# Optimization experiments

Measured on AMD Instinct MI355X. Metric: run time of the kernel, lower is better.

The kernel has to match this reference:

```python
import jax, jax.numpy as jnp
import numpy as np

N = 20000        # graph_node_num
C = 512          # cluster_num
E = 640000       # num edges (avg degree 32)
NFEAT = 128


def _gcn(x, W, b, edge_index, n):
    # PyG GCNConv: add self-loops, symmetric deg^-1/2 normalization, h = x @ W.T, bias after aggregation
    loop = jnp.arange(n, dtype=edge_index.dtype)
    src = jnp.concatenate([edge_index[0], loop])
    dst = jnp.concatenate([edge_index[1], loop])
    deg = jax.ops.segment_sum(jnp.ones_like(dst, x.dtype), dst, num_segments=n)
    dinv = jax.lax.rsqrt(jnp.maximum(deg, 1.0))  # deg >= 1 due to self-loops
    norm = dinv[src] * dinv[dst]                 # [E+n]
    h = x @ W.T                                  # [n, out]
    out = jax.ops.segment_sum(norm[:, None] * h[src], dst, num_segments=n)
    return out + b


def setup_inputs() -> dict:
    rng = np.random.default_rng(0)
    key = jax.random.key(0)
    edge = rng.integers(0, N, size=(2, E), dtype=np.int32)
    cluster = rng.integers(0, C, size=(N,), dtype=np.int32)
    # avg_pool coarsening of edge_index: remap to cluster ids, drop self-loops, coalesce (dedupe)
    cs, cd = cluster[edge[0]], cluster[edge[1]]
    m = cs != cd
    pairs = np.unique(cs[m].astype(np.int64) * C + cd[m].astype(np.int64))
    coarse_edge = np.stack([pairs // C, pairs % C]).astype(np.int32)

    ks = jax.random.split(key, 16)

    def w(k, o, i):
        return (jax.random.normal(k, (o, i), jnp.float32) / np.sqrt(i)).astype(jnp.float32)

    return {
        "x": jax.random.normal(ks[0], (N, NFEAT), jnp.float32),
        "W_G1": w(ks[1], 64, NFEAT), "b_G1": jnp.zeros((64,), jnp.float32),
        "Wf_G1": w(ks[2], 128, 64), "bf_G1": jnp.zeros((128,), jnp.float32),
        "W_G2": w(ks[3], 256, 128), "b_G2": jnp.zeros((256,), jnp.float32),
        "Wf_G2": w(ks[4], 256, 256), "bf_G2": jnp.zeros((256,), jnp.float32),
        "W_L1": w(ks[5], 128, 256), "b_L1": jnp.zeros((128,), jnp.float32),
        "Wf_L1": w(ks[6], 96, 128), "bf_L1": jnp.zeros((96,), jnp.float32),
        "W_L2": w(ks[7], 64, 96), "b_L2": jnp.zeros((64,), jnp.float32),
        "Wf_L2": w(ks[8], 32, 64), "bf_L2": jnp.zeros((32,), jnp.float32),
        "W_M1": w(ks[9], 16, 32), "b_M1": jnp.zeros((16,), jnp.float32),
        "Wf_M1": w(ks[10], 8, 16), "bf_M1": jnp.zeros((8,), jnp.float32),
        "W_O1": w(ks[11], 5, 8), "b_O1": jnp.zeros((5,), jnp.float32),
        "W_fcO": w(ks[12], 3 * N, 5 * C),  # fc_O1, bias=False
        "edge_index": jnp.asarray(edge),
        "cluster": jnp.asarray(cluster),
        "in_batch": jnp.zeros((N,), jnp.int32),
        "coarse_edge_index": jnp.asarray(coarse_edge),
    }


def reference(x, W_G1, b_G1, Wf_G1, bf_G1, W_G2, b_G2, Wf_G2, bf_G2,
              W_L1, b_L1, Wf_L1, bf_L1, W_L2, b_L2, Wf_L2, bf_L2,
              W_M1, b_M1, Wf_M1, bf_M1, W_O1, b_O1, W_fcO,
              edge_index, cluster, in_batch, coarse_edge_index):
    elu = jax.nn.elu
    x = elu(_gcn(x, W_G1, b_G1, edge_index, N))
    x = elu(x @ Wf_G1.T + bf_G1)
    x = elu(_gcn(x, W_G2, b_G2, edge_index, N))
    x = elu(x @ Wf_G2.T + bf_G2)
    # InstanceNorm(256), no batch arg -> single graph, per-channel over nodes, no affine
    mu = x.mean(axis=0)
    var = x.var(axis=0)
    y = (x - mu) * jax.lax.rsqrt(var + 1e-5)
    # avg_pool over clusters (batch_num=1 -> batch_cluster == cluster)
    bc = cluster + in_batch * C
    cnt = jax.ops.segment_sum(jnp.ones((N,), y.dtype), bc, num_segments=C)
    cx = jax.ops.segment_sum(y, bc, num_segments=C) / jnp.maximum(cnt, 1.0)[:, None]
    z = elu(_gcn(cx, W_L1, b_L1, coarse_edge_index, C))
    z = elu(z @ Wf_L1.T + bf_L1)
    z = elu(_gcn(z, W_L2, b_L2, coarse_edge_index, C))
    z = elu(z @ Wf_L2.T + bf_L2)
    z = elu(_gcn(z, W_M1, b_M1, coarse_edge_index, C))
    z = elu(z @ Wf_M1.T + bf_M1)
    g_feat = _gcn(z, W_O1, b_O1, coarse_edge_index, C).reshape(-1)  # [5*C]
    o_feat = W_fcO @ g_feat                                        # [3*N]
    return (g_feat, o_feat)
```

## Files before the change

kernel.cpp:

```cpp
#include <hip/hip_runtime.h>
#include <math.h>

#define NN 20000
#define CC 512

__device__ __forceinline__ float eluf(float x) { return x > 0.f ? x : __expf(x) - 1.f; }

__global__ void k_zero(float4* __restrict__ p, int n4) {
  int i = blockIdx.x * blockDim.x + threadIdx.x;
  if (i < n4) p[i] = make_float4(0.f, 0.f, 0.f, 0.f);
}

__global__ void k_count3(const int* __restrict__ dstF, int nF, int* __restrict__ cF,
                         const int* __restrict__ dstC, int nC, int* __restrict__ cC,
                         const int* __restrict__ clus, int nK, int* __restrict__ cK) {
  int i = blockIdx.x * blockDim.x + threadIdx.x;
  if (i < nF) { atomicAdd(&cF[dstF[i]], 1); return; }
  i -= nF;
  if (i < nC) { atomicAdd(&cC[dstC[i]], 1); return; }
  i -= nC;
  if (i < nK) atomicAdd(&cK[clus[i]], 1);
}

__global__ __launch_bounds__(1024) void k_scan3(
    const int* __restrict__ c0, int n0, int* __restrict__ r0, float* __restrict__ d0,
    const int* __restrict__ c1, int n1, int* __restrict__ r1, float* __restrict__ d1,
    const int* __restrict__ c2, int n2, int* __restrict__ r2) {
  const int* counts; int n; int* rowptr; float* dinv;
  if (blockIdx.x == 0) { counts = c0; n = n0; rowptr = r0; dinv = d0; }
  else if (blockIdx.x == 1) { counts = c1; n = n1; rowptr = r1; dinv = d1; }
  else { counts = c2; n = n2; rowptr = r2; dinv = nullptr; }
  __shared__ int part[1024];
  int tid = threadIdx.x;
  int chunk = (n + 1023) >> 10;
  int beg = tid * chunk;
  int fin = beg + chunk; if (fin > n) fin = n;
  int s = 0;
  for (int i = beg; i < fin; ++i) {
    int c = counts[i];
    s += c;
    if (dinv) dinv[i] = rsqrtf((float)(c + 1));
  }
  part[tid] = s;
  __syncthreads();
  for (int off = 1; off < 1024; off <<= 1) {
    int v = (tid >= off) ? part[tid - off] : 0;
    __syncthreads();
    part[tid] += v;
    __syncthreads();
  }
  int base = (tid == 0) ? 0 : part[tid - 1];
  for (int i = beg; i < fin; ++i) { rowptr[i] = base; base += counts[i]; }
  if (tid == 1023) rowptr[n] = part[1023];
}

__global__ void k_scatter3(
    const int* __restrict__ edgeF, int EF, const int* __restrict__ rowF, int* __restrict__ fillF,
    const float* __restrict__ dinvF, int* __restrict__ csrcF, float* __restrict__ cnormF,
    const int* __restrict__ edgeC, int EC, const int* __restrict__ rowC, int* __restrict__ fillC,
    const float* __restrict__ dinvC, int* __restrict__ csrcC, float* __restrict__ cnormC,
    const int* __restrict__ clus, int NK, const int* __restrict__ rowK, int* __restrict__ fillK,
    int* __restrict__ cnodes) {
  int i = blockIdx.x * blockDim.x + threadIdx.x;
  if (i < EF) {
    int d = edgeF[EF + i];
    int pos = rowF[d] + atomicAdd(&fillF[d], 1);
    int s = edgeF[i];
    csrcF[pos] = s;
    cnormF[pos] = dinvF[s] * dinvF[d];
    return;
  }
  i -= EF;
  if (i < EC) {
    int d = edgeC[EC + i];
    int pos = rowC[d] + atomicAdd(&fillC[d], 1);
    int s = edgeC[i];
    csrcC[pos] = s;
    cnormC[pos] = dinvC[s] * dinvC[d];
    return;
  }
  i -= EC;
  if (i < NK) {
    int d = clus[i];
    int pos = rowK[d] + atomicAdd(&fillK[d], 1);
    cnodes[pos] = i;
  }
}

__global__ __launch_bounds__(256) void k_gemm(const float* __restrict__ X,
                                              const float* __restrict__ W,
                                              const float* __restrict__ bias,
                                              float* __restrict__ Y,
                                              int nrows, int K, int outF, int act) {
  __shared__ float Xt[64][65];
  __shared__ float Wt[64][65];
  int row0 = blockIdx.x * 64;
  int col0 = blockIdx.y * 64;
  int tid = threadIdx.x;
  int cg = (tid & 15) * 4;
  int rg = (tid >> 4) * 4;
  float acc[4][4] = {};
  for (int kk = 0; kk < K; kk += 64) {
#pragma unroll
    for (int i = 0; i < 4; ++i) {
      int f = tid + 256 * i;
      int a = f >> 4;
      int kq = f & 15;
      int gk = kk + kq * 4;
      float4 xv = make_float4(0.f, 0.f, 0.f, 0.f);
      int gr = row0 + a;
      if (gr < nrows && gk < K) xv = *(const float4*)&X[(size_t)gr * K + gk];
      int kb = kq * 4;
      Xt[a][kb] = xv.x; Xt[a][kb + 1] = xv.y; Xt[a][kb + 2] = xv.z; Xt[a][kb + 3] = xv.w;
      float4 wv = make_float4(0.f, 0.f, 0.f, 0.f);
      int gc = col0 + a;
      if (gc < outF && gk < K) wv = *(const float4*)&W[(size_t)gc * K + gk];
      Wt[kb][a] = wv.x; Wt[kb + 1][a] = wv.y; Wt[kb + 2][a] = wv.z; Wt[kb + 3][a] = wv.w;
    }
    __syncthreads();
#pragma unroll 8
    for (int k = 0; k < 64; ++k) {
      float w0 = Wt[k][cg + 0], w1 = Wt[k][cg + 1], w2 = Wt[k][cg + 2], w3 = Wt[k][cg + 3];
      float x0 = Xt[rg + 0][k], x1 = Xt[rg + 1][k], x2 = Xt[rg + 2][k], x3 = Xt[rg + 3][k];
      acc[0][0] += x0 * w0; acc[0][1] += x0 * w1; acc[0][2] += x0 * w2; acc[0][3] += x0 * w3;
      acc[1][0] += x1 * w0; acc[1][1] += x1 * w1; acc[1][2] += x1 * w2; acc[1][3] += x1 * w3;
      acc[2][0] += x2 * w0; acc[2][1] += x2 * w1; acc[2][2] += x2 * w2; acc[2][3] += x2 * w3;
      acc[3][0] += x3 * w0; acc[3][1] += x3 * w1; acc[3][2] += x3 * w2; acc[3][3] += x3 * w3;
    }
    __syncthreads();
  }
#pragma unroll
  for (int i = 0; i < 4; ++i) {
    int gr = row0 + rg + i;
    if (gr >= nrows) continue;
#pragma unroll
    for (int j = 0; j < 4; ++j) {
      int gc = col0 + cg + j;
      if (gc >= outF) continue;
      float v = acc[i][j];
      if (bias) v += bias[gc];
      if (act) v = eluf(v);
      Y[(size_t)gr * outF + gc] = v;
    }
  }
}

__global__ __launch_bounds__(256) void k_gemm2(const float* __restrict__ X,
                                               const float* __restrict__ W,
                                               const float* __restrict__ bias,
                                               float* __restrict__ Y,
                                               int nrows, int K, int outF, int act) {
  __shared__ float Xt[32][132];
  __shared__ float Wt[32][68];
  int row0 = blockIdx.x * 128;
  int col0 = blockIdx.y * 64;
  int tid = threadIdx.x;
  int tc = (tid & 15) * 4;
  int tr = (tid >> 4) * 8;
  float acc[8][4] = {};
  for (int kk = 0; kk < K; kk += 32) {
#pragma unroll
    for (int i = 0; i < 4; ++i) {
      int f = tid + 256 * i;
      int r = f >> 3;
      int kq = f & 7;
      int gr = row0 + r;
      float4 v = make_float4(0.f, 0.f, 0.f, 0.f);
      if (gr < nrows) v = *(const float4*)&X[(size_t)gr * K + kk + kq * 4];
      int kb = kq * 4;
      Xt[kb][r] = v.x; Xt[kb + 1][r] = v.y; Xt[kb + 2][r] = v.z; Xt[kb + 3][r] = v.w;
    }
#pragma unroll
    for (int i = 0; i < 2; ++i) {
      int f = tid + 256 * i;
      int c = f >> 3;
      int kq = f & 7;
      int gc = col0 + c;
      float4 v = make_float4(0.f, 0.f, 0.f, 0.f);
      if (gc < outF) v = *(const float4*)&W[(size_t)gc * K + kk + kq * 4];
      int kb = kq * 4;
      Wt[kb][c] = v.x; Wt[kb + 1][c] = v.y; Wt[kb + 2][c] = v.z; Wt[kb + 3][c] = v.w;
    }
    __syncthreads();
#pragma unroll 8
    for (int k = 0; k < 32; ++k) {
      float4 w = *(const float4*)&Wt[k][tc];
      float4 xa = *(const float4*)&Xt[k][tr];
      float4 xb = *(const float4*)&Xt[k][tr + 4];
      float xs[8] = {xa.x, xa.y, xa.z, xa.w, xb.x, xb.y, xb.z, xb.w};
      float ws4[4] = {w.x, w.y, w.z, w.w};
#pragma unroll
      for (int i = 0; i < 8; ++i)
#pragma unroll
        for (int j = 0; j < 4; ++j) acc[i][j] += xs[i] * ws4[j];
    }
    __syncthreads();
  }
#pragma unroll
  for (int i = 0; i < 8; ++i) {
    int gr = row0 + tr + i;
    if (gr >= nrows) continue;
    int gc = col0 + tc;
    float4 v;
    v.x = acc[i][0]; v.y = acc[i][1]; v.z = acc[i][2]; v.w = acc[i][3];
    if (bias) { v.x += bias[gc]; v.y += bias[gc + 1]; v.z += bias[gc + 2]; v.w += bias[gc + 3]; }
    if (act) { v.x = eluf(v.x); v.y = eluf(v.y); v.z = eluf(v.z); v.w = eluf(v.w); }
    if (gc + 3 < outF) {
      *(float4*)&Y[(size_t)gr * outF + gc] = v;
    } else {
      float vs[4] = {v.x, v.y, v.z, v.w};
      for (int j = 0; j < 4; ++j)
        if (gc + j < outF) Y[(size_t)gr * outF + gc + j] = vs[j];
    }
  }
}

__global__ __launch_bounds__(256) void k_agg_fine64(
    const int* __restrict__ rowptr, const int* __restrict__ csrc, const float* __restrict__ cnorm,
    const float* __restrict__ h, const float* __restrict__ dinv, const float* __restrict__ bias,
    float* __restrict__ out, int n) {
  int w = blockIdx.x * 4 + (threadIdx.x >> 6);
  if (w >= n) return;
  int lane = threadIdx.x & 63;
  int start = rowptr[w], end = rowptr[w + 1];
  float acc = 0.f;
  int e = start;
  while (e < end && (e & 3)) { acc += cnorm[e] * h[(size_t)csrc[e] * 64 + lane]; ++e; }
  for (; e + 7 < end; e += 8) {
    int4 ia = *(const int4*)&csrc[e];
    int4 ib = *(const int4*)&csrc[e + 4];
    float4 na = *(const float4*)&cnorm[e];
    float4 nb = *(const float4*)&cnorm[e + 4];
    float v0 = h[(size_t)ia.x * 64 + lane];
    float v1 = h[(size_t)ia.y * 64 + lane];
    float v2 = h[(size_t)ia.z * 64 + lane];
    float v3 = h[(size_t)ia.w * 64 + lane];
    float v4 = h[(size_t)ib.x * 64 + lane];
    float v5 = h[(size_t)ib.y * 64 + lane];
    float v6 = h[(size_t)ib.z * 64 + lane];
    float v7 = h[(size_t)ib.w * 64 + lane];
    acc += na.x * v0 + na.y * v1 + na.z * v2 + na.w * v3 +
           nb.x * v4 + nb.y * v5 + nb.z * v6 + nb.w * v7;
  }
  for (; e < end; ++e) acc += cnorm[e] * h[(size_t)csrc[e] * 64 + lane];
  float dd = dinv[w]; dd *= dd;
  out[(size_t)w * 64 + lane] = eluf(acc + dd * h[(size_t)w * 64 + lane] + bias[lane]);
}

__global__ __launch_bounds__(256) void k_agg_fine128(
    const int* __restrict__ rowptr, const int* __restrict__ csrc, const float* __restrict__ cnorm,
    const float2* __restrict__ h2, const float* __restrict__ dinv,
    float2* __restrict__ out2, int n) {
  int w = blockIdx.x * 4 + (threadIdx.x >> 6);
  if (w >= n) return;
  int lane = threadIdx.x & 63;
  int start = rowptr[w], end = rowptr[w + 1];
  float ax = 0.f, ay = 0.f;
  int e = start;
  while (e < end && (e & 3)) {
    float nm = cnorm[e];
    float2 v = h2[(size_t)csrc[e] * 64 + lane];
    ax += nm * v.x; ay += nm * v.y; ++e;
  }
  for (; e + 7 < end; e += 8) {
    int4 ia = *(const int4*)&csrc[e];
    int4 ib = *(const int4*)&csrc[e + 4];
    float4 na = *(const float4*)&cnorm[e];
    float4 nb = *(const float4*)&cnorm[e + 4];
    float2 v0 = h2[(size_t)ia.x * 64 + lane];
    float2 v1 = h2[(size_t)ia.y * 64 + lane];
    float2 v2 = h2[(size_t)ia.z * 64 + lane];
    float2 v3 = h2[(size_t)ia.w * 64 + lane];
    float2 v4 = h2[(size_t)ib.x * 64 + lane];
    float2 v5 = h2[(size_t)ib.y * 64 + lane];
    float2 v6 = h2[(size_t)ib.z * 64 + lane];
    float2 v7 = h2[(size_t)ib.w * 64 + lane];
    ax += na.x * v0.x + na.y * v1.x + na.z * v2.x + na.w * v3.x +
          nb.x * v4.x + nb.y * v5.x + nb.z * v6.x + nb.w * v7.x;
    ay += na.x * v0.y + na.y * v1.y + na.z * v2.y + na.w * v3.y +
          nb.x * v4.y + nb.y * v5.y + nb.z * v6.y + nb.w * v7.y;
  }
  for (; e < end; ++e) {
    float nm = cnorm[e];
    float2 v = h2[(size_t)csrc[e] * 64 + lane];
    ax += nm * v.x; ay += nm * v.y;
  }
  float dd = dinv[w]; dd *= dd;
  float2 hw = h2[(size_t)w * 64 + lane];
  float2 o;
  o.x = ax + dd * hw.x;
  o.y = ay + dd * hw.y;
  out2[(size_t)w * 64 + lane] = o;
}

__global__ __launch_bounds__(256) void k_agg_coarse(int F,
    const int* __restrict__ rowptr, const int* __restrict__ csrc, const float* __restrict__ cnorm,
    const float* __restrict__ h, const float* __restrict__ dinv, const float* __restrict__ bias,
    float* __restrict__ out, int act) {
  int d = blockIdx.x;
  int lane = threadIdx.x & 63, wv = threadIdx.x >> 6;
  int start = rowptr[d], end = rowptr[d + 1];
  int cnt = end - start;
  int per = (cnt + 3) >> 2;
  int wbeg = start + wv * per;
  int wend = wbeg + per; if (wend > end) wend = end;
  float acc0 = 0.f, acc1 = 0.f;
  int e = wbeg;
  for (; e + 3 < wend; e += 4) {
    int s0 = csrc[e], s1 = csrc[e + 1], s2 = csrc[e + 2], s3 = csrc[e + 3];
    float n0 = cnorm[e], n1 = cnorm[e + 1], n2 = cnorm[e + 2], n3 = cnorm[e + 3];
    if (lane < F)
      acc0 += n0 * h[(size_t)s0 * F + lane] + n1 * h[(size_t)s1 * F + lane] +
              n2 * h[(size_t)s2 * F + lane] + n3 * h[(size_t)s3 * F + lane];
    if (lane + 64 < F)
      acc1 += n0 * h[(size_t)s0 * F + lane + 64] + n1 * h[(size_t)s1 * F + lane + 64] +
              n2 * h[(size_t)s2 * F + lane + 64] + n3 * h[(size_t)s3 * F + lane + 64];
  }
  for (; e < wend; ++e) {
    int s = csrc[e];
    float nm = cnorm[e];
    if (lane < F) acc0 += nm * h[(size_t)s * F + lane];
    if (lane + 64 < F) acc1 += nm * h[(size_t)s * F + lane + 64];
  }
  __shared__ float red[4][128];
  if (lane < F) red[wv][lane] = acc0;
  if (lane + 64 < F) red[wv][lane + 64] = acc1;
  __syncthreads();
  if (wv == 0) {
#pragma unroll 2
    for (int j = 0; j < 2; ++j) {
      int c = lane + j * 64;
      if (c < F) {
        float v = red[0][c] + red[1][c] + red[2][c] + red[3][c];
        float dd = dinv[d] * dinv[d];
        v += dd * h[(size_t)d * F + c] + bias[c];
        if (act) v = eluf(v);
        out[(size_t)d * F + c] = v;
      }
    }
  }
}

__global__ __launch_bounds__(256) void k_agg_coarse_fc2(int F,
    const int* __restrict__ rowptr, const int* __restrict__ csrc, const float* __restrict__ cnorm,
    const float* __restrict__ h, const float* __restrict__ dinv, const float* __restrict__ bias,
    const float* __restrict__ Wf, const float* __restrict__ bf, int outF2,
    const float* __restrict__ W2, int outF3,
    float* __restrict__ out) {
  int d = blockIdx.x;
  int lane = threadIdx.x & 63, wv = threadIdx.x >> 6;
  int start = rowptr[d], end = rowptr[d + 1];
  int cnt = end - start;
  int per = (cnt + 3) >> 2;
  int wbeg = start + wv * per;
  int wend = wbeg + per; if (wend > end) wend = end;
  float acc0 = 0.f, acc1 = 0.f;
  int e = wbeg;
  for (; e + 3 < wend; e += 4) {
    int s0 = csrc[e], s1 = csrc[e + 1], s2 = csrc[e + 2], s3 = csrc[e + 3];
    float n0 = cnorm[e], n1 = cnorm[e + 1], n2 = cnorm[e + 2], n3 = cnorm[e + 3];
    if (lane < F)
      acc0 += n0 * h[(size_t)s0 * F + lane] + n1 * h[(size_t)s1 * F + lane] +
              n2 * h[(size_t)s2 * F + lane] + n3 * h[(size_t)s3 * F + lane];
    if (lane + 64 < F)
      acc1 += n0 * h[(size_t)s0 * F + lane + 64] + n1 * h[(size_t)s1 * F + lane + 64] +
              n2 * h[(size_t)s2 * F + lane + 64] + n3 * h[(size_t)s3 * F + lane + 64];
  }
  for (; e < wend; ++e) {
    int s = csrc[e];
    float nm = cnorm[e];
    if (lane < F) acc0 += nm * h[(size_t)s * F + lane];
    if (lane + 64 < F) acc1 += nm * h[(size_t)s * F + lane + 64];
  }
  __shared__ float red[4][128];
  __shared__ __align__(16) float a_sh[128];
  __shared__ __align__(16) float z2_sh[96];
  if (lane < F) red[wv][lane] = acc0;
  if (lane + 64 < F) red[wv][lane + 64] = acc1;
  __syncthreads();
  if (wv == 0) {
#pragma unroll 2
    for (int j = 0; j < 2; ++j) {
      int c = lane + j * 64;
      if (c < F) {
        float v = red[0][c] + red[1][c] + red[2][c] + red[3][c];
        float dd = dinv[d] * dinv[d];
        a_sh[c] = eluf(v + dd * h[(size_t)d * F + c] + bias[c]);
      }
    }
  }
  __syncthreads();
  int j = threadIdx.x;
  if (j < outF2) {
    const float4* wr = (const float4*)(Wf + (size_t)j * F);
    const float4* ar = (const float4*)a_sh;
    float s = bf[j];
    for (int c = 0; c < (F >> 2); ++c) {
      float4 wv4 = wr[c];
      float4 av = ar[c];
      s += wv4.x * av.x + wv4.y * av.y + wv4.z * av.z + wv4.w * av.w;
    }
    z2_sh[j] = eluf(s);
  }
  __syncthreads();
  int m = threadIdx.x;
  if (m < outF3) {
    const float4* wr = (const float4*)(W2 + (size_t)m * outF2);
    const float4* zr = (const float4*)z2_sh;
    float s = 0.f;
    for (int c = 0; c < (outF2 >> 2); ++c) {
      float4 wv4 = wr[c];
      float4 zv = zr[c];
      s += wv4.x * zv.x + wv4.y * zv.y + wv4.z * zv.z + wv4.w * zv.w;
    }
    out[(size_t)d * outF3 + m] = s;
  }
}

__global__ __launch_bounds__(256) void k_chanstats(const float* __restrict__ x, int n,
                                                   float* __restrict__ s, float* __restrict__ s2) {
  int ch = threadIdx.x;
  float a = 0.f, b = 0.f;
  for (int r = blockIdx.x; r < n; r += gridDim.x) {
    float v = x[(size_t)r * 256 + ch];
    a += v;
    b += v * v;
  }
  atomicAdd(&s[ch], a);
  atomicAdd(&s2[ch], b);
}

__global__ __launch_bounds__(256) void k_pool(const float* __restrict__ x,
                                              const int* __restrict__ rowptr,
                                              const int* __restrict__ nodes,
                                              const float* __restrict__ sS,
                                              const float* __restrict__ sS2,
                                              float ninv,
                                              float* __restrict__ cx) {
  int c = blockIdx.x;
  int ch = threadIdx.x;
  float mu = sS[ch] * ninv;
  float var = sS2[ch] * ninv - mu * mu;
  float rstd = rsqrtf(var + 1e-5f);
  int start = rowptr[c], end = rowptr[c + 1];
  float s = 0.f;
  int i = start;
  for (; i + 3 < end; i += 4) {
    float v0 = x[(size_t)nodes[i] * 256 + ch];
    float v1 = x[(size_t)nodes[i + 1] * 256 + ch];
    float v2 = x[(size_t)nodes[i + 2] * 256 + ch];
    float v3 = x[(size_t)nodes[i + 3] * 256 + ch];
    s += v0 + v1 + v2 + v3;
  }
  for (; i < end; ++i) s += x[(size_t)nodes[i] * 256 + ch];
  int cnt = end - start; if (cnt < 1) cnt = 1;
  float v = s / (float)cnt;
  cx[(size_t)c * 256 + ch] = (v - mu) * rstd;
}

__global__ __launch_bounds__(256) void k_matvec(const float* __restrict__ W,
                                                const float* __restrict__ g,
                                                float* __restrict__ out, int M, int K) {
  __shared__ __align__(16) float gs[2560];
  for (int i = threadIdx.x; i < K; i += 256) gs[i] = g[i];
  __syncthreads();
  int lane = threadIdx.x & 63, wv = threadIdx.x >> 6;
#pragma unroll
  for (int rr = 0; rr < 4; ++rr) {
    int row = blockIdx.x * 16 + wv * 4 + rr;
    if (row >= M) break;
    const float4* Wr = (const float4*)(W + (size_t)row * K);
    float acc = 0.f;
#pragma unroll
    for (int it = 0; it < 10; ++it) {
      float4 w4 = Wr[it * 64 + lane];
      float4 g4 = *(const float4*)&gs[it * 256 + lane * 4];
      acc += w4.x * g4.x + w4.y * g4.y + w4.z * g4.z + w4.w * g4.w;
    }
#pragma unroll
    for (int off = 32; off; off >>= 1) acc += __shfl_down(acc, off, 64);
    if (lane == 0) out[row] = acc;
  }
}

extern "C" void kernel_launch(void* const* d_in, const int* in_sizes, int n_in,
                              void* d_out, int out_size, void* d_ws, size_t ws_size,
                              hipStream_t stream) {
  const float* x     = (const float*)d_in[0];
  const float* W_G1  = (const float*)d_in[1];
  const float* b_G1  = (const float*)d_in[2];
  const float* Wf_G1 = (const float*)d_in[3];
  const float* bf_G1 = (const float*)d_in[4];
  const float* W_G2  = (const float*)d_in[5];
  const float* b_G2  = (const float*)d_in[6];
  const float* Wf_G2 = (const float*)d_in[7];
  const float* bf_G2 = (const float*)d_in[8];
  const float* W_L1  = (const float*)d_in[9];
  const float* b_L1  = (const float*)d_in[10];
  const float* Wf_L1 = (const float*)d_in[11];
  const float* bf_L1 = (const float*)d_in[12];
  const float* W_L2  = (const float*)d_in[13];
  const float* b_L2  = (const float*)d_in[14];
  const float* Wf_L2 = (const float*)d_in[15];
  const float* bf_L2 = (const float*)d_in[16];
  const float* W_M1  = (const float*)d_in[17];
  const float* b_M1  = (const float*)d_in[18];
  const float* Wf_M1 = (const float*)d_in[19];
  const float* bf_M1 = (const float*)d_in[20];
  const float* W_O1  = (const float*)d_in[21];
  const float* b_O1  = (const float*)d_in[22];
  const float* W_fcO = (const float*)d_in[23];
  const int* edge    = (const int*)d_in[24];
  const int* cluster = (const int*)d_in[25];
  const int* cedge   = (const int*)d_in[27];

  const int E  = in_sizes[24] / 2;
  const int Ec = in_sizes[27] / 2;

  char* ws = (char*)d_ws;
  size_t off = 0;
  auto alloc = [&](size_t bytes) -> void* {
    void* p = ws + off;
    off = (off + bytes + 255) & ~(size_t)255;
    return p;
  };

  float* bufA = (float*)alloc((size_t)NN * 256 * 4);
  float* bufB = (float*)alloc((size_t)NN * 256 * 4);
  float* bufC = (float*)alloc((size_t)NN * 256 * 4);
  float* cx   = (float*)alloc((size_t)CC * 256 * 4);
  float* zA   = (float*)alloc((size_t)CC * 256 * 4);
  float* zB   = (float*)alloc((size_t)CC * 256 * 4);
  float* dinvF = (float*)alloc((size_t)NN * 4);
  float* dinvC = (float*)alloc((size_t)CC * 4);
  int* rowF  = (int*)alloc((size_t)(NN + 1) * 4);
  int* rowC  = (int*)alloc((size_t)(CC + 1) * 4);
  int* rowCl = (int*)alloc((size_t)(CC + 1) * 4);
  int* csrcF = (int*)alloc((size_t)E * 4);
  float* cnormF = (float*)alloc((size_t)E * 4);
  int* csrcC = (int*)alloc((size_t)Ec * 4);
  float* cnormC = (float*)alloc((size_t)Ec * 4);
  int* cnodes = (int*)alloc((size_t)NN * 4);
  size_t zoff = off;
  int* degF  = (int*)alloc((size_t)NN * 4);
  int* fillF = (int*)alloc((size_t)NN * 4);
  int* degC  = (int*)alloc((size_t)CC * 4);
  int* fillC = (int*)alloc((size_t)CC * 4);
  int* degCl = (int*)alloc((size_t)CC * 4);
  int* fillCl = (int*)alloc((size_t)CC * 4);
  float* chanS  = (float*)alloc(256 * 4);
  float* chanS2 = (float*)alloc(256 * 4);
  size_t zbytes = off - zoff;

  float* g_out = (float*)d_out;
  float* o_out = (float*)d_out + 2560;

  auto cdiv = [](int a, int b) { return (a + b - 1) / b; };

  k_zero<<<cdiv((int)(zbytes / 16), 256), 256, 0, stream>>>((float4*)(ws + zoff), (int)(zbytes / 16));

  k_count3<<<cdiv(E + Ec + NN, 256), 256, 0, stream>>>(edge + E, E, degF,
                                                       cedge + Ec, Ec, degC,
                                                       cluster, NN, degCl);
  k_scan3<<<3, 1024, 0, stream>>>(degF, NN, rowF, dinvF,
                                  degC, CC, rowC, dinvC,
                                  degCl, CC, rowCl);
  k_scatter3<<<cdiv(E + Ec + NN, 256), 256, 0, stream>>>(
      edge, E, rowF, fillF, dinvF, csrcF, cnormF,
      cedge, Ec, rowC, fillC, dinvC, csrcC, cnormC,
      cluster, NN, rowCl, fillCl, cnodes);

  k_gemm2<<<dim3(cdiv(NN, 128), 1), 256, 0, stream>>>(x, W_G1, nullptr, bufA, NN, 128, 64, 0);
  k_agg_fine64<<<NN / 4, 256, 0, stream>>>(rowF, csrcF, cnormF, bufA, dinvF, b_G1, bufC, NN);
  k_gemm2<<<dim3(cdiv(NN, 128), 2), 256, 0, stream>>>(bufC, Wf_G1, bf_G1, bufA, NN, 64, 128, 1);
  k_agg_fine128<<<NN / 4, 256, 0, stream>>>(rowF, csrcF, cnormF, (const float2*)bufA, dinvF,
                                            (float2*)bufC, NN);
  k_gemm2<<<dim3(cdiv(NN, 128), 4), 256, 0, stream>>>(bufC, W_G2, b_G2, bufB, NN, 128, 256, 1);
  k_gemm2<<<dim3(cdiv(NN, 128), 4), 256, 0, stream>>>(bufB, Wf_G2, bf_G2, bufA, NN, 256, 256, 1);

  k_chanstats<<<256, 256, 0, stream>>>(bufA, NN, chanS, chanS2);
  k_pool<<<CC, 256, 0, stream>>>(bufA, rowCl, cnodes, chanS, chanS2, 1.f / (float)NN, cx);

  k_gemm<<<dim3(8, 2), 256, 0, stream>>>(cx, W_L1, nullptr, zA, CC, 256, 128, 0);
  k_agg_coarse_fc2<<<CC, 256, 0, stream>>>(128, rowC, csrcC, cnormC, zA, dinvC, b_L1,
                                           Wf_L1, bf_L1, 96, W_L2, 64, zB);
  k_agg_coarse_fc2<<<CC, 256, 0, stream>>>(64, rowC, csrcC, cnormC, zB, dinvC, b_L2,
                                           Wf_L2, bf_L2, 32, W_M1, 16, zA);
  k_agg_coarse_fc2<<<CC, 256, 0, stream>>>(16, rowC, csrcC, cnormC, zA, dinvC, b_M1,
                                           Wf_M1, bf_M1, 8, W_O1, 5, zB);
  k_agg_coarse<<<CC, 256, 0, stream>>>(5, rowC, csrcC, cnormC, zB, dinvC, b_O1, g_out, 0);

  k_matvec<<<cdiv(3 * NN, 16), 256, 0, stream>>>(W_fcO, g_out, o_out, 3 * NN, 2560);
}
```

Baseline: 556.0 us.

## Split 128-wide fine aggregation into two passes and fuse pooling with L1 GEMM

The 128-feature fine aggregation now runs as two launches, each gathering one 64-column half of h, instead of one pass with float2 gathers. This shrinks the gathered working set per pass so it can stay resident in cache, at the price of reading the CSR indices and norms twice. Separately, the cluster pooling kernel now also computes the W_L1 projection per cluster row from shared memory, which removes the cx buffer and one tiny GEMM launch. Each pooling block re-reads all of W_L1 from global memory, and only half its threads do the matvec.

```diff
diff --git a/kernel.cpp b/kernel.cpp
--- a/kernel.cpp
+++ b/kernel.cpp
@@ -84,64 +84,6 @@
     int d = clus[i];
     int pos = rowK[d] + atomicAdd(&fillK[d], 1);
     cnodes[pos] = i;
-  }
-}
-
-__global__ __launch_bounds__(256) void k_gemm(const float* __restrict__ X,
-                                              const float* __restrict__ W,
-                                              const float* __restrict__ bias,
-                                              float* __restrict__ Y,
-                                              int nrows, int K, int outF, int act) {
-  __shared__ float Xt[64][65];
-  __shared__ float Wt[64][65];
-  int row0 = blockIdx.x * 64;
-  int col0 = blockIdx.y * 64;
-  int tid = threadIdx.x;
-  int cg = (tid & 15) * 4;
-  int rg = (tid >> 4) * 4;
-  float acc[4][4] = {};
-  for (int kk = 0; kk < K; kk += 64) {
-#pragma unroll
-    for (int i = 0; i < 4; ++i) {
-      int f = tid + 256 * i;
-      int a = f >> 4;
-      int kq = f & 15;
-      int gk = kk + kq * 4;
-      float4 xv = make_float4(0.f, 0.f, 0.f, 0.f);
-      int gr = row0 + a;
-      if (gr < nrows && gk < K) xv = *(const float4*)&X[(size_t)gr * K + gk];
-      int kb = kq * 4;
-      Xt[a][kb] = xv.x; Xt[a][kb + 1] = xv.y; Xt[a][kb + 2] = xv.z; Xt[a][kb + 3] = xv.w;
-      float4 wv = make_float4(0.f, 0.f, 0.f, 0.f);
-      int gc = col0 + a;
-      if (gc < outF && gk < K) wv = *(const float4*)&W[(size_t)gc * K + gk];
-      Wt[kb][a] = wv.x; Wt[kb + 1][a] = wv.y; Wt[kb + 2][a] = wv.z; Wt[kb + 3][a] = wv.w;
-    }
-    __syncthreads();
-#pragma unroll 8
-    for (int k = 0; k < 64; ++k) {
-      float w0 = Wt[k][cg + 0], w1 = Wt[k][cg + 1], w2 = Wt[k][cg + 2], w3 = Wt[k][cg + 3];
-      float x0 = Xt[rg + 0][k], x1 = Xt[rg + 1][k], x2 = Xt[rg + 2][k], x3 = Xt[rg + 3][k];
-      acc[0][0] += x0 * w0; acc[0][1] += x0 * w1; acc[0][2] += x0 * w2; acc[0][3] += x0 * w3;
-      acc[1][0] += x1 * w0; acc[1][1] += x1 * w1; acc[1][2] += x1 * w2; acc[1][3] += x1 * w3;
-      acc[2][0] += x2 * w0; acc[2][1] += x2 * w1; acc[2][2] += x2 * w2; acc[2][3] += x2 * w3;
-      acc[3][0] += x3 * w0; acc[3][1] += x3 * w1; acc[3][2] += x3 * w2; acc[3][3] += x3 * w3;
-    }
-    __syncthreads();
-  }
-#pragma unroll
-  for (int i = 0; i < 4; ++i) {
-    int gr = row0 + rg + i;
-    if (gr >= nrows) continue;
-#pragma unroll
-    for (int j = 0; j < 4; ++j) {
-      int gc = col0 + cg + j;
-      if (gc >= outF) continue;
-      float v = acc[i][j];
-      if (bias) v += bias[gc];
-      if (act) v = eluf(v);
-      Y[(size_t)gr * outF + gc] = v;
-    }
   }
 }
 
@@ -247,50 +189,37 @@
   out[(size_t)w * 64 + lane] = eluf(acc + dd * h[(size_t)w * 64 + lane] + bias[lane]);
 }
 
-__global__ __launch_bounds__(256) void k_agg_fine128(
+__global__ __launch_bounds__(256) void k_agg_fine128h(
     const int* __restrict__ rowptr, const int* __restrict__ csrc, const float* __restrict__ cnorm,
-    const float2* __restrict__ h2, const float* __restrict__ dinv,
-    float2* __restrict__ out2, int n) {
+    const float* __restrict__ h, const float* __restrict__ dinv,
+    float* __restrict__ out, int n, int half) {
   int w = blockIdx.x * 4 + (threadIdx.x >> 6);
   if (w >= n) return;
   int lane = threadIdx.x & 63;
+  const float* hh = h + half * 64 + lane;
   int start = rowptr[w], end = rowptr[w + 1];
-  float ax = 0.f, ay = 0.f;
+  float acc = 0.f;
   int e = start;
-  while (e < end && (e & 3)) {
-    float nm = cnorm[e];
-    float2 v = h2[(size_t)csrc[e] * 64 + lane];
-    ax += nm * v.x; ay += nm * v.y; ++e;
-  }
+  while (e < end && (e & 3)) { acc += cnorm[e] * hh[(size_t)csrc[e] * 128]; ++e; }
   for (; e + 7 < end; e += 8) {
     int4 ia = *(const int4*)&csrc[e];
     int4 ib = *(const int4*)&csrc[e + 4];
     float4 na = *(const float4*)&cnorm[e];
     float4 nb = *(const float4*)&cnorm[e + 4];
-    float2 v0 = h2[(size_t)ia.x * 64 + lane];
-    float2 v1 = h2[(size_t)ia.y * 64 + lane];
-    float2 v2 = h2[(size_t)ia.z * 64 + lane];
-    float2 v3 = h2[(size_t)ia.w * 64 + lane];
-    float2 v4 = h2[(size_t)ib.x * 64 + lane];
-    float2 v5 = h2[(size_t)ib.y * 64 + lane];
-    float2 v6 = h2[(size_t)ib.z * 64 + lane];
-    float2 v7 = h2[(size_t)ib.w * 64 + lane];
-    ax += na.x * v0.x + na.y * v1.x + na.z * v2.x + na.w * v3.x +
-          nb.x * v4.x + nb.y * v5.x + nb.z * v6.x + nb.w * v7.x;
-    ay += na.x * v0.y + na.y * v1.y + na.z * v2.y + na.w * v3.y +
-          nb.x * v4.y + nb.y * v5.y + nb.z * v6.y + nb.w * v7.y;
-  }
-  for (; e < end; ++e) {
-    float nm = cnorm[e];
-    float2 v = h2[(size_t)csrc[e] * 64 + lane];
-    ax += nm * v.x; ay += nm * v.y;
-  }
+    float v0 = hh[(size_t)ia.x * 128];
+    float v1 = hh[(size_t)ia.y * 128];
+    float v2 = hh[(size_t)ia.z * 128];
+    float v3 = hh[(size_t)ia.w * 128];
+    float v4 = hh[(size_t)ib.x * 128];
+    float v5 = hh[(size_t)ib.y * 128];
+    float v6 = hh[(size_t)ib.z * 128];
+    float v7 = hh[(size_t)ib.w * 128];
+    acc += na.x * v0 + na.y * v1 + na.z * v2 + na.w * v3 +
+           nb.x * v4 + nb.y * v5 + nb.z * v6 + nb.w * v7;
+  }
+  for (; e < end; ++e) acc += cnorm[e] * hh[(size_t)csrc[e] * 128];
   float dd = dinv[w]; dd *= dd;
-  float2 hw = h2[(size_t)w * 64 + lane];
-  float2 o;
-  o.x = ax + dd * hw.x;
-  o.y = ay + dd * hw.y;
-  out2[(size_t)w * 64 + lane] = o;
+  out[(size_t)w * 128 + half * 64 + lane] = acc + dd * hh[(size_t)w * 128];
 }
 
 __global__ __launch_bounds__(256) void k_agg_coarse(int F,
@@ -430,15 +359,17 @@
   atomicAdd(&s2[ch], b);
 }
 
-__global__ __launch_bounds__(256) void k_pool(const float* __restrict__ x,
-                                              const int* __restrict__ rowptr,
-                                              const int* __restrict__ nodes,
-                                              const float* __restrict__ sS,
-                                              const float* __restrict__ sS2,
-                                              float ninv,
-                                              float* __restrict__ cx) {
+__global__ __launch_bounds__(256) void k_pool_gemm(const float* __restrict__ x,
+                                                   const int* __restrict__ rowptr,
+                                                   const int* __restrict__ nodes,
+                                                   const float* __restrict__ sS,
+                                                   const float* __restrict__ sS2,
+                                                   float ninv,
+                                                   const float* __restrict__ W,
+                                                   float* __restrict__ t) {
   int c = blockIdx.x;
   int ch = threadIdx.x;
+  __shared__ __align__(16) float a_sh[256];
   float mu = sS[ch] * ninv;
   float var = sS2[ch] * ninv - mu * mu;
   float rstd = rsqrtf(var + 1e-5f);
@@ -454,8 +385,21 @@
   }
   for (; i < end; ++i) s += x[(size_t)nodes[i] * 256 + ch];
   int cnt = end - start; if (cnt < 1) cnt = 1;
-  float v = s / (float)cnt;
-  cx[(size_t)c * 256 + ch] = (v - mu) * rstd;
+  a_sh[ch] = (s / (float)cnt - mu) * rstd;
+  __syncthreads();
+  int j = threadIdx.x;
+  if (j < 128) {
+    const float4* wr = (const float4*)(W + (size_t)j * 256);
+    const float4* ar = (const float4*)a_sh;
+    float acc = 0.f;
+#pragma unroll 8
+    for (int q = 0; q < 64; ++q) {
+      float4 w4 = wr[q];
+      float4 av = ar[q];
+      acc += w4.x * av.x + w4.y * av.y + w4.z * av.z + w4.w * av.w;
+    }
+    t[(size_t)c * 128 + j] = acc;
+  }
 }
 
 __global__ __launch_bounds__(256) void k_matvec(const float* __restrict__ W,
@@ -528,7 +472,6 @@
   float* bufA = (float*)alloc((size_t)NN * 256 * 4);
   float* bufB = (float*)alloc((size_t)NN * 256 * 4);
   float* bufC = (float*)alloc((size_t)NN * 256 * 4);
-  float* cx   = (float*)alloc((size_t)CC * 256 * 4);
   float* zA   = (float*)alloc((size_t)CC * 256 * 4);
   float* zB   = (float*)alloc((size_t)CC * 256 * 4);
   float* dinvF = (float*)alloc((size_t)NN * 4);
@@ -573,15 +516,15 @@
   k_gemm2<<<dim3(cdiv(NN, 128), 1), 256, 0, stream>>>(x, W_G1, nullptr, bufA, NN, 128, 64, 0);
   k_agg_fine64<<<NN / 4, 256, 0, stream>>>(rowF, csrcF, cnormF, bufA, dinvF, b_G1, bufC, NN);
   k_gemm2<<<dim3(cdiv(NN, 128), 2), 256, 0, stream>>>(bufC, Wf_G1, bf_G1, bufA, NN, 64, 128, 1);
-  k_agg_fine128<<<NN / 4, 256, 0, stream>>>(rowF, csrcF, cnormF, (const float2*)bufA, dinvF,
-                                            (float2*)bufC, NN);
+  k_agg_fine128h<<<NN / 4, 256, 0, stream>>>(rowF, csrcF, cnormF, bufA, dinvF, bufC, NN, 0);
+  k_agg_fine128h<<<NN / 4, 256, 0, stream>>>(rowF, csrcF, cnormF, bufA, dinvF, bufC, NN, 1);
   k_gemm2<<<dim3(cdiv(NN, 128), 4), 256, 0, stream>>>(bufC, W_G2, b_G2, bufB, NN, 128, 256, 1);
   k_gemm2<<<dim3(cdiv(NN, 128), 4), 256, 0, stream>>>(bufB, Wf_G2, bf_G2, bufA, NN, 256, 256, 1);
 
   k_chanstats<<<256, 256, 0, stream>>>(bufA, NN, chanS, chanS2);
-  k_pool<<<CC, 256, 0, stream>>>(bufA, rowCl, cnodes, chanS, chanS2, 1.f / (float)NN, cx);
-
-  k_gemm<<<dim3(8, 2), 256, 0, stream>>>(cx, W_L1, nullptr, zA, CC, 256, 128, 0);
+  k_pool_gemm<<<CC, 256, 0, stream>>>(bufA, rowCl, cnodes, chanS, chanS2, 1.f / (float)NN,
+                                      W_L1, zA);
+
   k_agg_coarse_fc2<<<CC, 256, 0, stream>>>(128, rowC, csrcC, cnormC, zA, dinvC, b_L1,
                                            Wf_L1, bf_L1, 96, W_L2, 64, zB);
   k_agg_coarse_fc2<<<CC, 256, 0, stream>>>(64, rowC, csrcC, cnormC, zB, dinvC, b_L2,
```

Result: no change. 548.3 us (median of 2 runs) (-1.4%).
